# Optimization experiments

Hardware: AMD Instinct MI355X
Metric: run time of the kernel (lower is better)

The kernel has to match this reference:

```python
import jax, jax.numpy as jnp
import numpy as np

B, S, K, D = 2048, 32, 1024, 64
DECAY = 0.9
LOG_2PI = float(np.log(2.0 * np.pi))


def _gmm_log_probs(slots, mu, log_sigma):
    """log N(slots | mu_k, sigma_k) summed over feature dim -> [B, S, K].

    Expanded quadratic form avoids materializing the [B,S,K,D] broadcast:
    -0.5 * sum_d (x-mu)^2/var - sum_d log sigma - 0.5*D*log(2*pi)
    """
    inv_var = jnp.exp(-2.0 * log_sigma)                      # [K, D]
    x2 = jnp.einsum('bsd,kd->bsk', slots * slots, inv_var)    # sum x^2/var
    xm = jnp.einsum('bsd,kd->bsk', slots, mu * inv_var)       # sum x*mu/var
    m2 = jnp.sum(mu * mu * inv_var, axis=-1)                  # [K]
    const = jnp.sum(log_sigma, axis=-1) + 0.5 * D * LOG_2PI   # [K]
    return -0.5 * (x2 - 2.0 * xm + m2) - const


def setup_inputs() -> dict:
    key = jax.random.key(0)
    k0, k1, k2, k3 = jax.random.split(key, 4)
    return {
        'slots': jax.random.normal(k0, (B, S, D), dtype=jnp.float32),
        'mu': jax.random.normal(k1, (K, D), dtype=jnp.float32),
        'log_sigma': jax.random.normal(k2, (K, D), dtype=jnp.float32),
        'log_prior': jnp.zeros((K,), dtype=jnp.float32),
        'z': jax.random.normal(k3, (B, S, D), dtype=jnp.float32),
    }


def reference(slots, mu, log_sigma, log_prior, z):
    sigma = jnp.exp(log_sigma)                                # [K, D]
    log_probs = _gmm_log_probs(slots, mu, log_sigma)          # [B, S, K]
    responsibilities = jax.nn.softmax(log_probs, axis=-1)     # [B, S, K]
    # argmax of responsibilities == argmax of log_probs (softmax is monotone)
    assignments = jnp.argmax(log_probs, axis=-1)              # [B, S] int
    new_slots = mu[assignments] + sigma[assignments] * z      # [B, S, D]
    log_likelihood = jnp.take_along_axis(
        log_probs, assignments[..., None], axis=-1)[..., 0]   # [B, S]
    # EMA prior update (non-trainable buffer in the original module)
    new_log_prior = (DECAY * jax.nn.softmax(log_prior)
                     + (1.0 - DECAY) * jax.nn.softmax(
                         jnp.sum(responsibilities, axis=(0, 1))))
    return new_slots, log_likelihood, new_log_prior
```

## Files before the change

kernel.cpp:

```cpp
#include <hip/hip_runtime.h>
#include <math.h>

#define KK 1024
#define DD 64
#define BS 65536
#define TM 32
#define NBLK (BS/TM)
#define NTHR 512
#define LN_2PI 1.8378770664093453f
#define DECAY 0.9f
#define APAD 136

typedef _Float16 f16x8 __attribute__((ext_vector_type(8)));
typedef _Float16 f16x4 __attribute__((ext_vector_type(4)));
typedef float f32x16 __attribute__((ext_vector_type(16)));

#define BH_OFF   0
#define BL_OFF   65536
#define C_OFF    131072
#define SIG_OFF  (C_OFF + KK)
#define RESP_OFF (SIG_OFF + KK*DD)

__global__ __launch_bounds__(64) void prep_kernel(
    const float* __restrict__ mu, const float* __restrict__ log_sigma,
    float* __restrict__ ws) {
  int k = blockIdx.x;
  int d = threadIdx.x;
  float ls = log_sigma[k*DD + d];
  float m  = mu[k*DD + d];
  float iv = expf(-2.0f*ls);
  _Float16* Bh = (_Float16*)(ws + BH_OFF);
  _Float16* Bl = (_Float16*)(ws + BL_OFF);
  {
    float w0 = -0.5f*iv;
    _Float16 hh = (_Float16)w0;
    Bh[((size_t)(d >> 3)*KK + k)*8 + (d & 7)] = hh;
    Bl[((size_t)(d >> 3)*KK + k)*8 + (d & 7)] = (_Float16)(w0 - (float)hh);
  }
  {
    float w1 = m*iv;
    _Float16 hh = (_Float16)w1;
    int dd = 64 + d;
    Bh[((size_t)(dd >> 3)*KK + k)*8 + (dd & 7)] = hh;
    Bl[((size_t)(dd >> 3)*KK + k)*8 + (dd & 7)] = (_Float16)(w1 - (float)hh);
  }
  ws[SIG_OFF + k*DD + d] = expf(ls);
  float t1 = m*m*iv;
  float t2 = ls;
  #pragma unroll
  for (int off = 32; off; off >>= 1) {
    t1 += __shfl_xor(t1, off);
    t2 += __shfl_xor(t2, off);
  }
  if (d == 0) ws[C_OFF + k] = -0.5f*t1 - t2 - 32.0f*LN_2PI;
}

__global__ __launch_bounds__(512, 4) void main_kernel(
    const float* __restrict__ slots, const float* __restrict__ mu,
    const float* __restrict__ z, const float* __restrict__ ws,
    float* __restrict__ out_slots, float* __restrict__ out_ll,
    float* __restrict__ resp_g) {
  __shared__ _Float16 Ah[TM][APAD];
  __shared__ _Float16 Al[TM][APAD];
  __shared__ float mxl[TM][8];
  __shared__ float sml[TM][8];
  __shared__ float gm_l[TM];
  __shared__ float inv_l[TM];
  __shared__ int   am_l[TM];

  const int t    = threadIdx.x;
  const int lane = t & 63;
  const int w    = t >> 6;
  const int h    = lane >> 5;
  const int lc   = lane & 31;
  const int R0   = blockIdx.x * TM;

  {
    int row = t >> 4;
    int dp  = (t & 15) * 4;
    float4 v = *(const float4*)(slots + (size_t)(R0 + row)*DD + dp);
    float f[4] = {v.x, v.y, v.z, v.w};
    f16x4 sqh, sql, sh, sl;
    #pragma unroll
    for (int j = 0; j < 4; ++j) {
      float sq = f[j]*f[j];
      _Float16 h1 = (_Float16)sq;
      sqh[j] = h1; sql[j] = (_Float16)(sq - (float)h1);
      _Float16 h2 = (_Float16)f[j];
      sh[j] = h2;  sl[j]  = (_Float16)(f[j] - (float)h2);
    }
    *(f16x4*)&Ah[row][dp]      = sqh;
    *(f16x4*)&Al[row][dp]      = sql;
    *(f16x4*)&Ah[row][64 + dp] = sh;
    *(f16x4*)&Al[row][64 + dp] = sl;
  }
  if (t < TM) am_l[t] = 0x7fffffff;
  __syncthreads();

  const f16x8* BH = (const f16x8*)(ws + BH_OFF);
  const f16x8* BL = (const f16x8*)(ws + BL_OFF);
  const int col0 = (w << 7) + lc;
  const f16x8* pH = BH + (size_t)h*KK + col0;
  const f16x8* pL = BL + (size_t)h*KK + col0;

  f32x16 acc[4];
  {
    const float* Cc = ws + C_OFF;
    #pragma unroll
    for (int ct = 0; ct < 4; ++ct) {
      float cv = Cc[col0 + ct*32];
      f32x16 ini;
      #pragma unroll
      for (int j = 0; j < 16; ++j) ini[j] = cv;
      acc[ct] = ini;
    }
  }

  #pragma unroll
  for (int s = 0; s < 8; ++s) {
    f16x8 ah = *(const f16x8*)&Ah[lc][s*16 + h*8];
    f16x8 al = *(const f16x8*)&Al[lc][s*16 + h*8];
    #pragma unroll
    for (int ct = 0; ct < 4; ++ct) {
      f16x8 bh = pH[(size_t)s*2*KK + ct*32];
      f16x8 bl = pL[(size_t)s*2*KK + ct*32];
      acc[ct] = __builtin_amdgcn_mfma_f32_32x32x16_f16(ah, bh, acc[ct], 0, 0, 0);
      acc[ct] = __builtin_amdgcn_mfma_f32_32x32x16_f16(ah, bl, acc[ct], 0, 0, 0);
      acc[ct] = __builtin_amdgcn_mfma_f32_32x32x16_f16(al, bh, acc[ct], 0, 0, 0);
    }
  }

  #pragma unroll
  for (int q = 0; q < 16; ++q) {
    float m = fmaxf(fmaxf(acc[0][q], acc[1][q]), fmaxf(acc[2][q], acc[3][q]));
    #pragma unroll
    for (int off = 1; off < 32; off <<= 1)
      m = fmaxf(m, __shfl_xor(m, off));
    if (lc == 0) mxl[(q&3) + 8*(q>>2) + 4*h][w] = m;
  }
  __syncthreads();

  if (t < TM) {
    float m = mxl[t][0];
    #pragma unroll
    for (int g = 1; g < 8; ++g) m = fmaxf(m, mxl[t][g]);
    gm_l[t] = m;
    out_ll[R0 + t] = m;
  }
  __syncthreads();

  #pragma unroll
  for (int q = 0; q < 16; ++q) {
    const int row = (q&3) + 8*(q>>2) + 4*h;
    const float gm = gm_l[row];
    int cand = 0x7fffffff;
    #pragma unroll
    for (int ct = 3; ct >= 0; --ct)
      if (acc[ct][q] == gm) cand = col0 + ct*32;
    if (cand != 0x7fffffff) atomicMin(&am_l[row], cand);
    float sacc = 0.0f;
    #pragma unroll
    for (int ct = 0; ct < 4; ++ct) {
      float e = __expf(acc[ct][q] - gm);
      acc[ct][q] = e;
      sacc += e;
    }
    #pragma unroll
    for (int off = 1; off < 32; off <<= 1) sacc += __shfl_xor(sacc, off);
    if (lc == 0) sml[row][w] = sacc;
  }
  __syncthreads();
  if (t < TM) {
    float ssum = 0.0f;
    #pragma unroll
    for (int g = 0; g < 8; ++g) ssum += sml[t][g];
    inv_l[t] = 1.0f / ssum;
  }
  __syncthreads();

  {
    float rc[4] = {0.0f, 0.0f, 0.0f, 0.0f};
    #pragma unroll
    for (int q = 0; q < 16; ++q) {
      int row = (q&3) + 8*(q>>2) + 4*h;
      float inv = inv_l[row];
      #pragma unroll
      for (int ct = 0; ct < 4; ++ct) rc[ct] += acc[ct][q] * inv;
    }
    #pragma unroll
    for (int ct = 0; ct < 4; ++ct) rc[ct] += __shfl_xor(rc[ct], 32);
    if (lane < 32) {
      #pragma unroll
      for (int ct = 0; ct < 4; ++ct) atomicAdd(resp_g + col0 + ct*32, rc[ct]);
    }
  }

  {
    const int frow = t >> 4;
    const int fdp  = (t & 15) * 4;
    const int fa   = am_l[frow];
    float4 fz = *(const float4*)(z  + (size_t)(R0 + frow)*DD + fdp);
    float4 fm = *(const float4*)(mu + (size_t)fa*DD + fdp);
    float4 fs = *(const float4*)(ws + SIG_OFF + (size_t)fa*DD + fdp);
    float4 o;
    o.x = fmaf(fs.x, fz.x, fm.x); o.y = fmaf(fs.y, fz.y, fm.y);
    o.z = fmaf(fs.z, fz.z, fm.z); o.w = fmaf(fs.w, fz.w, fm.w);
    *(float4*)(out_slots + (size_t)(R0 + frow)*DD + fdp) = o;
  }
}

__device__ __forceinline__ float block_max_1024(float v, float* red) {
  #pragma unroll
  for (int off = 32; off; off >>= 1) v = fmaxf(v, __shfl_xor(v, off));
  int wave = threadIdx.x >> 6, lane = threadIdx.x & 63;
  if (lane == 0) red[wave] = v;
  __syncthreads();
  float m = red[0];
  #pragma unroll
  for (int w = 1; w < 16; ++w) m = fmaxf(m, red[w]);
  __syncthreads();
  return m;
}

__device__ __forceinline__ float block_sum_1024(float v, float* red) {
  #pragma unroll
  for (int off = 32; off; off >>= 1) v += __shfl_xor(v, off);
  int wave = threadIdx.x >> 6, lane = threadIdx.x & 63;
  if (lane == 0) red[wave] = v;
  __syncthreads();
  float s = 0.0f;
  #pragma unroll
  for (int w = 0; w < 16; ++w) s += red[w];
  __syncthreads();
  return s;
}

__global__ __launch_bounds__(1024) void finalize_kernel(
    const float* __restrict__ log_prior, const float* __restrict__ resp_g,
    float* __restrict__ out_prior) {
  __shared__ float red[16];
  int t = threadIdx.x;
  float lp = log_prior[t];
  float rs = resp_g[t];

  float m1 = block_max_1024(lp, red);
  float e1 = __expf(lp - m1);
  float s1 = block_sum_1024(e1, red);

  float m2 = block_max_1024(rs, red);
  float e2 = __expf(rs - m2);
  float s2 = block_sum_1024(e2, red);

  out_prior[t] = DECAY * (e1 / s1) + (1.0f - DECAY) * (e2 / s2);
}

extern "C" void kernel_launch(void* const* d_in, const int* in_sizes, int n_in,
                              void* d_out, int out_size, void* d_ws, size_t ws_size,
                              hipStream_t stream) {
  const float* slots     = (const float*)d_in[0];
  const float* mu        = (const float*)d_in[1];
  const float* log_sigma = (const float*)d_in[2];
  const float* log_prior = (const float*)d_in[3];
  const float* z         = (const float*)d_in[4];

  float* out       = (float*)d_out;
  float* out_slots = out;
  float* out_ll    = out + (size_t)BS*DD;
  float* out_prior = out + (size_t)BS*DD + BS;
  float* ws        = (float*)d_ws;

  hipMemsetAsync(ws + RESP_OFF, 0, KK*sizeof(float), stream);
  prep_kernel<<<KK, 64, 0, stream>>>(mu, log_sigma, ws);
  main_kernel<<<NBLK, NTHR, 0, stream>>>(slots, mu, z, ws, out_slots, out_ll,
                                         ws + RESP_OFF);
  finalize_kernel<<<1, 1024, 0, stream>>>(log_prior, ws + RESP_OFF, out_prior);
}
```

Measured before the change: 115.3 us.

## Switch main kernel to 16-row tiles using 16x16x32 MFMA

Halves the row tile from 32 to 16 and replaces the 32x32x16 MFMA with 16x16x32, giving each wave 8 column tiles of 16 instead of 4 of 32. The reductions, argmax, softmax and responsibility accumulation are reindexed to the new accumulator layout. Occupancy hint rises from 4 to 6 blocks. The aim is more blocks and less register pressure, but every block now reloads the whole B matrix for half as many rows, doubling B traffic from L2, and only half the threads do the load and output phases.

```diff
diff --git a/kernel.cpp b/kernel.cpp
--- a/kernel.cpp
+++ b/kernel.cpp
@@ -4,7 +4,7 @@
 #define KK 1024
 #define DD 64
 #define BS 65536
-#define TM 32
+#define TM 16
 #define NBLK (BS/TM)
 #define NTHR 512
 #define LN_2PI 1.8378770664093453f
@@ -13,7 +13,7 @@
 
 typedef _Float16 f16x8 __attribute__((ext_vector_type(8)));
 typedef _Float16 f16x4 __attribute__((ext_vector_type(4)));
-typedef float f32x16 __attribute__((ext_vector_type(16)));
+typedef float f32x4 __attribute__((ext_vector_type(4)));
 
 #define BH_OFF   0
 #define BL_OFF   65536
@@ -55,7 +55,7 @@
   if (d == 0) ws[C_OFF + k] = -0.5f*t1 - t2 - 32.0f*LN_2PI;
 }
 
-__global__ __launch_bounds__(512, 4) void main_kernel(
+__global__ __launch_bounds__(512, 6) void main_kernel(
     const float* __restrict__ slots, const float* __restrict__ mu,
     const float* __restrict__ z, const float* __restrict__ ws,
     float* __restrict__ out_slots, float* __restrict__ out_ll,
@@ -71,11 +71,11 @@
   const int t    = threadIdx.x;
   const int lane = t & 63;
   const int w    = t >> 6;
-  const int h    = lane >> 5;
-  const int lc   = lane & 31;
+  const int kg   = lane >> 4;
+  const int lc   = lane & 15;
   const int R0   = blockIdx.x * TM;
 
-  {
+  if (t < 256) {
     int row = t >> 4;
     int dp  = (t & 15) * 4;
     float4 v = *(const float4*)(slots + (size_t)(R0 + row)*DD + dp);
@@ -100,43 +100,42 @@
   const f16x8* BH = (const f16x8*)(ws + BH_OFF);
   const f16x8* BL = (const f16x8*)(ws + BL_OFF);
   const int col0 = (w << 7) + lc;
-  const f16x8* pH = BH + (size_t)h*KK + col0;
-  const f16x8* pL = BL + (size_t)h*KK + col0;
-
-  f32x16 acc[4];
+  const f16x8* pH = BH + (size_t)kg*KK + col0;
+  const f16x8* pL = BL + (size_t)kg*KK + col0;
+
+  f32x4 acc[8];
   {
     const float* Cc = ws + C_OFF;
     #pragma unroll
-    for (int ct = 0; ct < 4; ++ct) {
-      float cv = Cc[col0 + ct*32];
-      f32x16 ini;
-      #pragma unroll
-      for (int j = 0; j < 16; ++j) ini[j] = cv;
-      acc[ct] = ini;
-    }
-  }
-
-  #pragma unroll
-  for (int s = 0; s < 8; ++s) {
-    f16x8 ah = *(const f16x8*)&Ah[lc][s*16 + h*8];
-    f16x8 al = *(const f16x8*)&Al[lc][s*16 + h*8];
-    #pragma unroll
-    for (int ct = 0; ct < 4; ++ct) {
-      f16x8 bh = pH[(size_t)s*2*KK + ct*32];
-      f16x8 bl = pL[(size_t)s*2*KK + ct*32];
-      acc[ct] = __builtin_amdgcn_mfma_f32_32x32x16_f16(ah, bh, acc[ct], 0, 0, 0);
-      acc[ct] = __builtin_amdgcn_mfma_f32_32x32x16_f16(ah, bl, acc[ct], 0, 0, 0);
-      acc[ct] = __builtin_amdgcn_mfma_f32_32x32x16_f16(al, bh, acc[ct], 0, 0, 0);
-    }
-  }
-
-  #pragma unroll
-  for (int q = 0; q < 16; ++q) {
-    float m = fmaxf(fmaxf(acc[0][q], acc[1][q]), fmaxf(acc[2][q], acc[3][q]));
-    #pragma unroll
-    for (int off = 1; off < 32; off <<= 1)
+    for (int ct = 0; ct < 8; ++ct) {
+      float cv = Cc[col0 + ct*16];
+      acc[ct] = (f32x4){cv, cv, cv, cv};
+    }
+  }
+
+  #pragma unroll
+  for (int s = 0; s < 4; ++s) {
+    f16x8 ah = *(const f16x8*)&Ah[lc][s*32 + kg*8];
+    f16x8 al = *(const f16x8*)&Al[lc][s*32 + kg*8];
+    #pragma unroll
+    for (int ct = 0; ct < 8; ++ct) {
+      f16x8 bh = pH[(size_t)s*4*KK + ct*16];
+      f16x8 bl = pL[(size_t)s*4*KK + ct*16];
+      acc[ct] = __builtin_amdgcn_mfma_f32_16x16x32_f16(ah, bh, acc[ct], 0, 0, 0);
+      acc[ct] = __builtin_amdgcn_mfma_f32_16x16x32_f16(ah, bl, acc[ct], 0, 0, 0);
+      acc[ct] = __builtin_amdgcn_mfma_f32_16x16x32_f16(al, bh, acc[ct], 0, 0, 0);
+    }
+  }
+
+  #pragma unroll
+  for (int q = 0; q < 4; ++q) {
+    float m = acc[0][q];
+    #pragma unroll
+    for (int ct = 1; ct < 8; ++ct) m = fmaxf(m, acc[ct][q]);
+    #pragma unroll
+    for (int off = 1; off < 16; off <<= 1)
       m = fmaxf(m, __shfl_xor(m, off));
-    if (lc == 0) mxl[(q&3) + 8*(q>>2) + 4*h][w] = m;
+    if (lc == 0) mxl[kg*4 + q][w] = m;
   }
   __syncthreads();
 
@@ -150,23 +149,23 @@
   __syncthreads();
 
   #pragma unroll
-  for (int q = 0; q < 16; ++q) {
-    const int row = (q&3) + 8*(q>>2) + 4*h;
+  for (int q = 0; q < 4; ++q) {
+    const int row = kg*4 + q;
     const float gm = gm_l[row];
     int cand = 0x7fffffff;
     #pragma unroll
-    for (int ct = 3; ct >= 0; --ct)
-      if (acc[ct][q] == gm) cand = col0 + ct*32;
+    for (int ct = 7; ct >= 0; --ct)
+      if (acc[ct][q] == gm) cand = col0 + ct*16;
     if (cand != 0x7fffffff) atomicMin(&am_l[row], cand);
     float sacc = 0.0f;
     #pragma unroll
-    for (int ct = 0; ct < 4; ++ct) {
+    for (int ct = 0; ct < 8; ++ct) {
       float e = __expf(acc[ct][q] - gm);
       acc[ct][q] = e;
       sacc += e;
     }
     #pragma unroll
-    for (int off = 1; off < 32; off <<= 1) sacc += __shfl_xor(sacc, off);
+    for (int off = 1; off < 16; off <<= 1) sacc += __shfl_xor(sacc, off);
     if (lc == 0) sml[row][w] = sacc;
   }
   __syncthreads();
@@ -179,23 +178,28 @@
   __syncthreads();
 
   {
-    float rc[4] = {0.0f, 0.0f, 0.0f, 0.0f};
-    #pragma unroll
-    for (int q = 0; q < 16; ++q) {
-      int row = (q&3) + 8*(q>>2) + 4*h;
-      float inv = inv_l[row];
+    float rc[8];
+    #pragma unroll
+    for (int ct = 0; ct < 8; ++ct) rc[ct] = 0.0f;
+    #pragma unroll
+    for (int q = 0; q < 4; ++q) {
+      float inv = inv_l[kg*4 + q];
       #pragma unroll
-      for (int ct = 0; ct < 4; ++ct) rc[ct] += acc[ct][q] * inv;
-    }
-    #pragma unroll
-    for (int ct = 0; ct < 4; ++ct) rc[ct] += __shfl_xor(rc[ct], 32);
-    if (lane < 32) {
+      for (int ct = 0; ct < 8; ++ct) rc[ct] += acc[ct][q] * inv;
+    }
+    #pragma unroll
+    for (int ct = 0; ct < 8; ++ct) {
+      rc[ct] += __shfl_xor(rc[ct], 16);
+      rc[ct] += __shfl_xor(rc[ct], 32);
+    }
+    if (lane < 16) {
       #pragma unroll
-      for (int ct = 0; ct < 4; ++ct) atomicAdd(resp_g + col0 + ct*32, rc[ct]);
-    }
-  }
-
-  {
+      for (int ct = 0; ct < 8; ++ct)
+        atomicAdd(resp_g + (w << 7) + ct*16 + lane, rc[ct]);
+    }
+  }
+
+  if (t < 256) {
     const int frow = t >> 4;
     const int fdp  = (t & 15) * 4;
     const int fa   = am_l[frow];
```

Result: slower. 166.1 us (+44.1%).

## Double row tile to 64 with 1024-thread blocks and 2x2 MFMA tiles per wave

Applied to the files above, without the earlier changes.

Each block now handles 64 rows with 16 waves, and each wave computes a 64x64 output tile made of 2 row groups by 2 column groups. Each B fragment loaded from global memory now feeds two row groups, which cuts B-operand traffic per row in half. It also halves the number of blocks and the global atomicAdds into the responsibility sums. The costs are larger blocks and more accumulator registers per wave. The launch_bounds hint of 1024 threads with 4 blocks per CU is very tight and may force register spills or lower occupancy.

```diff
diff --git a/kernel.cpp b/kernel.cpp
--- a/kernel.cpp
+++ b/kernel.cpp
@@ -4,9 +4,9 @@
 #define KK 1024
 #define DD 64
 #define BS 65536
-#define TM 32
+#define TM 64
 #define NBLK (BS/TM)
-#define NTHR 512
+#define NTHR 1024
 #define LN_2PI 1.8378770664093453f
 #define DECAY 0.9f
 #define APAD 136
@@ -55,15 +55,15 @@
   if (d == 0) ws[C_OFF + k] = -0.5f*t1 - t2 - 32.0f*LN_2PI;
 }
 
-__global__ __launch_bounds__(512, 4) void main_kernel(
+__global__ __launch_bounds__(1024, 4) void main_kernel(
     const float* __restrict__ slots, const float* __restrict__ mu,
     const float* __restrict__ z, const float* __restrict__ ws,
     float* __restrict__ out_slots, float* __restrict__ out_ll,
     float* __restrict__ resp_g) {
   __shared__ _Float16 Ah[TM][APAD];
   __shared__ _Float16 Al[TM][APAD];
-  __shared__ float mxl[TM][8];
-  __shared__ float sml[TM][8];
+  __shared__ float mxl[TM][16];
+  __shared__ float sml[TM][16];
   __shared__ float gm_l[TM];
   __shared__ float inv_l[TM];
   __shared__ int   am_l[TM];
@@ -99,99 +99,109 @@
 
   const f16x8* BH = (const f16x8*)(ws + BH_OFF);
   const f16x8* BL = (const f16x8*)(ws + BL_OFF);
-  const int col0 = (w << 7) + lc;
+  const int col0 = (w << 6) + lc;
   const f16x8* pH = BH + (size_t)h*KK + col0;
   const f16x8* pL = BL + (size_t)h*KK + col0;
 
-  f32x16 acc[4];
+  f32x16 acc[2][2];
   {
     const float* Cc = ws + C_OFF;
     #pragma unroll
-    for (int ct = 0; ct < 4; ++ct) {
+    for (int ct = 0; ct < 2; ++ct) {
       float cv = Cc[col0 + ct*32];
       f32x16 ini;
       #pragma unroll
       for (int j = 0; j < 16; ++j) ini[j] = cv;
-      acc[ct] = ini;
+      acc[0][ct] = ini; acc[1][ct] = ini;
     }
   }
 
   #pragma unroll
   for (int s = 0; s < 8; ++s) {
-    f16x8 ah = *(const f16x8*)&Ah[lc][s*16 + h*8];
-    f16x8 al = *(const f16x8*)&Al[lc][s*16 + h*8];
-    #pragma unroll
-    for (int ct = 0; ct < 4; ++ct) {
+    f16x8 ah0 = *(const f16x8*)&Ah[lc     ][s*16 + h*8];
+    f16x8 al0 = *(const f16x8*)&Al[lc     ][s*16 + h*8];
+    f16x8 ah1 = *(const f16x8*)&Ah[32 + lc][s*16 + h*8];
+    f16x8 al1 = *(const f16x8*)&Al[32 + lc][s*16 + h*8];
+    #pragma unroll
+    for (int ct = 0; ct < 2; ++ct) {
       f16x8 bh = pH[(size_t)s*2*KK + ct*32];
       f16x8 bl = pL[(size_t)s*2*KK + ct*32];
-      acc[ct] = __builtin_amdgcn_mfma_f32_32x32x16_f16(ah, bh, acc[ct], 0, 0, 0);
-      acc[ct] = __builtin_amdgcn_mfma_f32_32x32x16_f16(ah, bl, acc[ct], 0, 0, 0);
-      acc[ct] = __builtin_amdgcn_mfma_f32_32x32x16_f16(al, bh, acc[ct], 0, 0, 0);
-    }
-  }
-
-  #pragma unroll
-  for (int q = 0; q < 16; ++q) {
-    float m = fmaxf(fmaxf(acc[0][q], acc[1][q]), fmaxf(acc[2][q], acc[3][q]));
-    #pragma unroll
-    for (int off = 1; off < 32; off <<= 1)
-      m = fmaxf(m, __shfl_xor(m, off));
-    if (lc == 0) mxl[(q&3) + 8*(q>>2) + 4*h][w] = m;
+      acc[0][ct] = __builtin_amdgcn_mfma_f32_32x32x16_f16(ah0, bh, acc[0][ct], 0, 0, 0);
+      acc[1][ct] = __builtin_amdgcn_mfma_f32_32x32x16_f16(ah1, bh, acc[1][ct], 0, 0, 0);
+      acc[0][ct] = __builtin_amdgcn_mfma_f32_32x32x16_f16(ah0, bl, acc[0][ct], 0, 0, 0);
+      acc[1][ct] = __builtin_amdgcn_mfma_f32_32x32x16_f16(ah1, bl, acc[1][ct], 0, 0, 0);
+      acc[0][ct] = __builtin_amdgcn_mfma_f32_32x32x16_f16(al0, bh, acc[0][ct], 0, 0, 0);
+      acc[1][ct] = __builtin_amdgcn_mfma_f32_32x32x16_f16(al1, bh, acc[1][ct], 0, 0, 0);
+    }
+  }
+
+  #pragma unroll
+  for (int rg = 0; rg < 2; ++rg) {
+    #pragma unroll
+    for (int q = 0; q < 16; ++q) {
+      float m = fmaxf(acc[rg][0][q], acc[rg][1][q]);
+      #pragma unroll
+      for (int off = 1; off < 32; off <<= 1)
+        m = fmaxf(m, __shfl_xor(m, off));
+      if (lc == 0) mxl[rg*32 + (q&3) + 8*(q>>2) + 4*h][w] = m;
+    }
   }
   __syncthreads();
 
   if (t < TM) {
     float m = mxl[t][0];
     #pragma unroll
-    for (int g = 1; g < 8; ++g) m = fmaxf(m, mxl[t][g]);
+    for (int g = 1; g < 16; ++g) m = fmaxf(m, mxl[t][g]);
     gm_l[t] = m;
     out_ll[R0 + t] = m;
   }
   __syncthreads();
 
   #pragma unroll
-  for (int q = 0; q < 16; ++q) {
-    const int row = (q&3) + 8*(q>>2) + 4*h;
-    const float gm = gm_l[row];
-    int cand = 0x7fffffff;
-    #pragma unroll
-    for (int ct = 3; ct >= 0; --ct)
-      if (acc[ct][q] == gm) cand = col0 + ct*32;
-    if (cand != 0x7fffffff) atomicMin(&am_l[row], cand);
-    float sacc = 0.0f;
-    #pragma unroll
-    for (int ct = 0; ct < 4; ++ct) {
-      float e = __expf(acc[ct][q] - gm);
-      acc[ct][q] = e;
-      sacc += e;
-    }
-    #pragma unroll
-    for (int off = 1; off < 32; off <<= 1) sacc += __shfl_xor(sacc, off);
-    if (lc == 0) sml[row][w] = sacc;
+  for (int rg = 0; rg < 2; ++rg) {
+    #pragma unroll
+    for (int q = 0; q < 16; ++q) {
+      const int row = rg*32 + (q&3) + 8*(q>>2) + 4*h;
+      const float gm = gm_l[row];
+      int cand = 0x7fffffff;
+      #pragma unroll
+      for (int ct = 1; ct >= 0; --ct)
+        if (acc[rg][ct][q] == gm) cand = col0 + ct*32;
+      if (cand != 0x7fffffff) atomicMin(&am_l[row], cand);
+      float e0 = __expf(acc[rg][0][q] - gm);
+      float e1 = __expf(acc[rg][1][q] - gm);
+      acc[rg][0][q] = e0; acc[rg][1][q] = e1;
+      float sacc = e0 + e1;
+      #pragma unroll
+      for (int off = 1; off < 32; off <<= 1) sacc += __shfl_xor(sacc, off);
+      if (lc == 0) sml[row][w] = sacc;
+    }
   }
   __syncthreads();
   if (t < TM) {
     float ssum = 0.0f;
     #pragma unroll
-    for (int g = 0; g < 8; ++g) ssum += sml[t][g];
+    for (int g = 0; g < 16; ++g) ssum += sml[t][g];
     inv_l[t] = 1.0f / ssum;
   }
   __syncthreads();
 
   {
-    float rc[4] = {0.0f, 0.0f, 0.0f, 0.0f};
-    #pragma unroll
-    for (int q = 0; q < 16; ++q) {
-      int row = (q&3) + 8*(q>>2) + 4*h;
-      float inv = inv_l[row];
-      #pragma unroll
-      for (int ct = 0; ct < 4; ++ct) rc[ct] += acc[ct][q] * inv;
-    }
-    #pragma unroll
-    for (int ct = 0; ct < 4; ++ct) rc[ct] += __shfl_xor(rc[ct], 32);
+    float rc[2] = {0.0f, 0.0f};
+    #pragma unroll
+    for (int rg = 0; rg < 2; ++rg) {
+      #pragma unroll
+      for (int q = 0; q < 16; ++q) {
+        float inv = inv_l[rg*32 + (q&3) + 8*(q>>2) + 4*h];
+        rc[0] += acc[rg][0][q] * inv;
+        rc[1] += acc[rg][1][q] * inv;
+      }
+    }
+    rc[0] += __shfl_xor(rc[0], 32);
+    rc[1] += __shfl_xor(rc[1], 32);
     if (lane < 32) {
-      #pragma unroll
-      for (int ct = 0; ct < 4; ++ct) atomicAdd(resp_g + col0 + ct*32, rc[ct]);
+      atomicAdd(resp_g + (w << 6) + lane,      rc[0]);
+      atomicAdd(resp_g + (w << 6) + 32 + lane, rc[1]);
     }
   }
 
```

Measured after the change: 136.0 us. 1.18x slower.

## Transpose MFMA output layout so row reductions stay in registers

Applied to the files above, without the earlier changes.

Swaps the MFMA operands so each lane holds one slot row across all its accumulator registers. The per-row max, argmax and softmax sum then become in-register loops with a single cross-half shuffle, replacing per-row 32-lane shuffle trees. The per-component constant now comes from a shared-memory copy added after the matmul. The trade-off is the column-wise responsibility sum: it now needs a 5-step shuffle reduction over all 64 accumulator values plus an extra shared-memory buffer and barrier before the global atomics.

```diff
diff --git a/kernel.cpp b/kernel.cpp
--- a/kernel.cpp
+++ b/kernel.cpp
@@ -14,6 +14,8 @@
 typedef _Float16 f16x8 __attribute__((ext_vector_type(8)));
 typedef _Float16 f16x4 __attribute__((ext_vector_type(4)));
 typedef float f32x16 __attribute__((ext_vector_type(16)));
+
+#define CLT(q) (((q) & 3) + 8 * ((q) >> 2))
 
 #define BH_OFF   0
 #define BL_OFF   65536
@@ -62,6 +64,8 @@
     float* __restrict__ resp_g) {
   __shared__ _Float16 Ah[TM][APAD];
   __shared__ _Float16 Al[TM][APAD];
+  __shared__ float cl[KK];
+  __shared__ float resl[KK];
   __shared__ float mxl[TM][8];
   __shared__ float sml[TM][8];
   __shared__ float gm_l[TM];
@@ -75,6 +79,13 @@
   const int lc   = lane & 31;
   const int R0   = blockIdx.x * TM;
 
+  const f16x8* BH = (const f16x8*)(ws + BH_OFF);
+  const f16x8* BL = (const f16x8*)(ws + BL_OFF);
+  const int col0 = (w << 7) + lc;
+  const f16x8* pH = BH + (size_t)h*KK + col0;
+  const f16x8* pL = BL + (size_t)h*KK + col0;
+  const int colbase = (w << 7) + 4*h;
+
   {
     int row = t >> 4;
     int dp  = (t & 15) * 4;
@@ -94,27 +105,14 @@
     *(f16x4*)&Ah[row][64 + dp] = sh;
     *(f16x4*)&Al[row][64 + dp] = sl;
   }
+  cl[t]       = ws[C_OFF + t];
+  cl[t + 512] = ws[C_OFF + t + 512];
   if (t < TM) am_l[t] = 0x7fffffff;
   __syncthreads();
 
-  const f16x8* BH = (const f16x8*)(ws + BH_OFF);
-  const f16x8* BL = (const f16x8*)(ws + BL_OFF);
-  const int col0 = (w << 7) + lc;
-  const f16x8* pH = BH + (size_t)h*KK + col0;
-  const f16x8* pL = BL + (size_t)h*KK + col0;
-
   f32x16 acc[4];
-  {
-    const float* Cc = ws + C_OFF;
-    #pragma unroll
-    for (int ct = 0; ct < 4; ++ct) {
-      float cv = Cc[col0 + ct*32];
-      f32x16 ini;
-      #pragma unroll
-      for (int j = 0; j < 16; ++j) ini[j] = cv;
-      acc[ct] = ini;
-    }
-  }
+  #pragma unroll
+  for (int ct = 0; ct < 4; ++ct) acc[ct] = (f32x16)(0.0f);
 
   #pragma unroll
   for (int s = 0; s < 8; ++s) {
@@ -124,19 +122,27 @@
     for (int ct = 0; ct < 4; ++ct) {
       f16x8 bh = pH[(size_t)s*2*KK + ct*32];
       f16x8 bl = pL[(size_t)s*2*KK + ct*32];
-      acc[ct] = __builtin_amdgcn_mfma_f32_32x32x16_f16(ah, bh, acc[ct], 0, 0, 0);
-      acc[ct] = __builtin_amdgcn_mfma_f32_32x32x16_f16(ah, bl, acc[ct], 0, 0, 0);
-      acc[ct] = __builtin_amdgcn_mfma_f32_32x32x16_f16(al, bh, acc[ct], 0, 0, 0);
-    }
-  }
-
-  #pragma unroll
-  for (int q = 0; q < 16; ++q) {
-    float m = fmaxf(fmaxf(acc[0][q], acc[1][q]), fmaxf(acc[2][q], acc[3][q]));
-    #pragma unroll
-    for (int off = 1; off < 32; off <<= 1)
-      m = fmaxf(m, __shfl_xor(m, off));
-    if (lc == 0) mxl[(q&3) + 8*(q>>2) + 4*h][w] = m;
+      acc[ct] = __builtin_amdgcn_mfma_f32_32x32x16_f16(bh, ah, acc[ct], 0, 0, 0);
+      acc[ct] = __builtin_amdgcn_mfma_f32_32x32x16_f16(bl, ah, acc[ct], 0, 0, 0);
+      acc[ct] = __builtin_amdgcn_mfma_f32_32x32x16_f16(bh, al, acc[ct], 0, 0, 0);
+    }
+  }
+
+  #pragma unroll
+  for (int ct = 0; ct < 4; ++ct)
+    #pragma unroll
+    for (int q = 0; q < 16; ++q)
+      acc[ct][q] += cl[colbase + ct*32 + CLT(q)];
+
+  {
+    float m = acc[0][0];
+    #pragma unroll
+    for (int ct = 0; ct < 4; ++ct)
+      #pragma unroll
+      for (int q = 0; q < 16; ++q)
+        m = fmaxf(m, acc[ct][q]);
+    m = fmaxf(m, __shfl_xor(m, 32));
+    if (lane < 32) mxl[lane][w] = m;
   }
   __syncthreads();
 
@@ -149,51 +155,62 @@
   }
   __syncthreads();
 
-  #pragma unroll
-  for (int q = 0; q < 16; ++q) {
-    const int row = (q&3) + 8*(q>>2) + 4*h;
-    const float gm = gm_l[row];
+  {
+    const float gm = gm_l[lc];
     int cand = 0x7fffffff;
     #pragma unroll
     for (int ct = 3; ct >= 0; --ct)
-      if (acc[ct][q] == gm) cand = col0 + ct*32;
-    if (cand != 0x7fffffff) atomicMin(&am_l[row], cand);
-    float sacc = 0.0f;
-    #pragma unroll
-    for (int ct = 0; ct < 4; ++ct) {
-      float e = __expf(acc[ct][q] - gm);
-      acc[ct][q] = e;
-      sacc += e;
-    }
-    #pragma unroll
-    for (int off = 1; off < 32; off <<= 1) sacc += __shfl_xor(sacc, off);
-    if (lc == 0) sml[row][w] = sacc;
+      #pragma unroll
+      for (int q = 15; q >= 0; --q)
+        if (acc[ct][q] == gm) cand = colbase + ct*32 + CLT(q);
+    if (cand != 0x7fffffff) atomicMin(&am_l[lc], cand);
+    float ssum = 0.0f;
+    #pragma unroll
+    for (int ct = 0; ct < 4; ++ct)
+      #pragma unroll
+      for (int q = 0; q < 16; ++q) {
+        float e = __expf(acc[ct][q] - gm);
+        acc[ct][q] = e;
+        ssum += e;
+      }
+    ssum += __shfl_xor(ssum, 32);
+    if (lane < 32) sml[lane][w] = ssum;
   }
   __syncthreads();
   if (t < TM) {
-    float ssum = 0.0f;
-    #pragma unroll
-    for (int g = 0; g < 8; ++g) ssum += sml[t][g];
-    inv_l[t] = 1.0f / ssum;
-  }
-  __syncthreads();
-
-  {
-    float rc[4] = {0.0f, 0.0f, 0.0f, 0.0f};
-    #pragma unroll
-    for (int q = 0; q < 16; ++q) {
-      int row = (q&3) + 8*(q>>2) + 4*h;
-      float inv = inv_l[row];
-      #pragma unroll
-      for (int ct = 0; ct < 4; ++ct) rc[ct] += acc[ct][q] * inv;
-    }
-    #pragma unroll
-    for (int ct = 0; ct < 4; ++ct) rc[ct] += __shfl_xor(rc[ct], 32);
-    if (lane < 32) {
-      #pragma unroll
-      for (int ct = 0; ct < 4; ++ct) atomicAdd(resp_g + col0 + ct*32, rc[ct]);
-    }
-  }
+    float s = 0.0f;
+    #pragma unroll
+    for (int g = 0; g < 8; ++g) s += sml[t][g];
+    inv_l[t] = 1.0f / s;
+  }
+  __syncthreads();
+
+  {
+    const float inv = inv_l[lc];
+    #pragma unroll
+    for (int ct = 0; ct < 4; ++ct)
+      #pragma unroll
+      for (int q = 0; q < 16; ++q)
+        acc[ct][q] *= inv;
+    #pragma unroll
+    for (int off = 1; off < 32; off <<= 1) {
+      #pragma unroll
+      for (int ct = 0; ct < 4; ++ct)
+        #pragma unroll
+        for (int q = 0; q < 16; ++q)
+          acc[ct][q] += __shfl_xor(acc[ct][q], off);
+    }
+    if (lc == 0) {
+      #pragma unroll
+      for (int ct = 0; ct < 4; ++ct)
+        #pragma unroll
+        for (int q = 0; q < 16; ++q)
+          resl[colbase + ct*32 + CLT(q)] = acc[ct][q];
+    }
+  }
+  __syncthreads();
+  atomicAdd(resp_g + t,       resl[t]);
+  atomicAdd(resp_g + t + 512, resl[t + 512]);
 
   {
     const int frow = t >> 4;
```

After: 132.7 us. +15.1%, slower.
